# Kernel optimization log

Measured on AMD Instinct MI355X. Metric: run time of the kernel, lower is better.

The kernel has to match this reference:

```python
import jax, jax.numpy as jnp
import numpy as np

N = 512   # speakers
M = 64    # samples per speaker
D = 768   # embedding dim
EPS = 1e-8  # torch F.cosine_similarity eps


def setup_inputs() -> dict:
    key = jax.random.key(0)
    k1, = jax.random.split(key, 1)
    speaker_vectors = jax.random.normal(k1, (N * M, D), dtype=jnp.float32)
    w = jnp.asarray(10.0, dtype=jnp.float32)
    b = jnp.asarray(-5.0, dtype=jnp.float32)
    return {"speaker_vectors": speaker_vectors, "w": w, "b": b}


def _cosine(a, b):
    # torch F.cosine_similarity: a.b / (max(|a|,eps) * max(|b|,eps)), over last dim
    na = jnp.maximum(jnp.linalg.norm(a, axis=-1), EPS)
    nb = jnp.maximum(jnp.linalg.norm(b, axis=-1), EPS)
    return jnp.sum(a * b, axis=-1) / (na * nb)


def reference(speaker_vectors, w, b):
    x = speaker_vectors.reshape(N, M, D)            # [N, M, D]
    sums = x.sum(axis=1)                            # [N, D]
    centroids = sums / M                            # [N, D]
    excl = (sums[:, None, :] - x) / (M - 1)         # exclusive centroids [N, M, D]

    # cosine sim of every centroid against every sample: [N_centroid, N_spk, M]
    xn = jnp.maximum(jnp.linalg.norm(x, axis=-1), EPS)          # [N, M]
    cn = jnp.maximum(jnp.linalg.norm(centroids, axis=-1), EPS)  # [N]
    dots = jnp.einsum('nd,imd->nim', centroids, x)              # [N, N, M]
    S = w * (dots / (cn[:, None, None] * xn[None])) + b         # [N, N, M]

    # same-speaker entries use the leave-one-out centroid
    S_same = w * _cosine(excl, x) + b               # [N, M]
    idx = jnp.arange(N)
    S = S.at[idx, idx].set(S_same)                  # overwrite diagonal block

    # L_j = -S_same_j + log sum_n exp(S[n, j])
    L = -S_same + jax.scipy.special.logsumexp(S, axis=0)  # [N, M]
    return L.sum()
```

## Files before the change

kernel.cpp:

```cpp
#include <hip/hip_runtime.h>
#include <hip/hip_bf16.h>
#include <math.h>

#define EPS 1e-8f

typedef __attribute__((ext_vector_type(2))) unsigned long ulongx2;
typedef __attribute__((ext_vector_type(4))) float floatx4;
typedef unsigned char uchar_t;

#define GPTR(p) ((const __attribute__((address_space(1))) void*)(p))
#define LPTR(p) ((__attribute__((address_space(3))) void*)(p))

__device__ __forceinline__ unsigned int pk4(float a, float b, float c, float d) {
  int v = __builtin_amdgcn_cvt_pk_fp8_f32(a, b, 0, false);
  v = __builtin_amdgcn_cvt_pk_fp8_f32(c, d, v, true);
  return (unsigned int)v;
}

__global__ __launch_bounds__(512, 4) void kA(const float* __restrict__ x,
    uchar_t* __restrict__ xbf8fm, float* __restrict__ sums_f32,
    float* __restrict__ ss, float* __restrict__ rcn,
    float* __restrict__ xx, float* __restrict__ rxn,
    const float* __restrict__ wp) {
  const int n = blockIdx.x;
  const int t = threadIdx.x;
  const int wv = t >> 6, l = t & 63;
  __shared__ uchar_t xs[64][776];
  __shared__ float rqp[64][65];
  __shared__ float red8[8];

  float4 cs[3] = {{0,0,0,0},{0,0,0,0},{0,0,0,0}};
  for (int c = 0; c < 2; ++c) {
    float4 v[4][3];
#pragma unroll
    for (int rr = 0; rr < 4; ++rr) {
      const int r = wv * 8 + c * 4 + rr;
      const float* rp = x + ((size_t)n * 64 + r) * 768 + l * 4;
#pragma unroll
      for (int q = 0; q < 3; ++q) v[rr][q] = *(const float4*)(rp + q * 256);
    }
#pragma unroll
    for (int rr = 0; rr < 4; ++rr) {
      const int r = wv * 8 + c * 4 + rr;
      float rq = 0.f;
#pragma unroll
      for (int q = 0; q < 3; ++q) {
        const float4 u = v[rr][q];
        *(unsigned int*)&xs[r][l * 4 + q * 256] = pk4(u.x, u.y, u.z, u.w);
        rq += u.x*u.x + u.y*u.y + u.z*u.z + u.w*u.w;
        cs[q].x += u.x; cs[q].y += u.y; cs[q].z += u.z; cs[q].w += u.w;
      }
      rqp[r][l] = rq;
    }
  }
  __syncthreads();

  {
    const int gg = wv >> 1;
    const int half = wv & 1;
    const int g = n * 4 + gg;
#pragma unroll
    for (int ksi = 0; ksi < 6; ++ksi) {
      const int ks = half * 6 + ksi;
      const uchar_t* sp = &xs[gg * 16 + (l & 15)][ks * 64 + (l >> 4) * 8];
      uint2 lo = *(const uint2*)sp;
      uint2 hi = *(const uint2*)(sp + 32);
      uint4 outv = {lo.x, lo.y, hi.x, hi.y};
      *(uint4*)(xbf8fm + (size_t)((g * 12 + ks) * 64 + l) * 16) = outv;
    }
  }

  {
    const int r = t >> 3;
    const int o = (t & 7) * 8;
    float s = 0.f;
#pragma unroll
    for (int i = 0; i < 8; ++i) s += rqp[r][o + i];
    s += __shfl_xor(s, 1, 64);
    s += __shfl_xor(s, 2, 64);
    s += __shfl_xor(s, 4, 64);
    if ((t & 7) == 0) {
      const int j = n * 64 + r;
      xx[j] = s;
      rxn[j] = 1.0f / fmaxf(sqrtf(s), EPS);
    }
  }
  __syncthreads();

  float (*csum)[768] = (float (*)[768])&xs[0][0];
#pragma unroll
  for (int q = 0; q < 3; ++q)
    *(floatx4*)&csum[wv][l * 4 + q * 256] = (floatx4){cs[q].x, cs[q].y, cs[q].z, cs[q].w};
  __syncthreads();

  float lss = 0.f;
  {
    const int c0 = t;
    float s0 = 0.f;
#pragma unroll
    for (int w = 0; w < 8; ++w) s0 += csum[w][c0];
    sums_f32[(size_t)n * 768 + c0] = s0;
    lss += s0 * s0;
    if (t < 256) {
      const int c1 = 512 + t;
      float s1 = 0.f;
#pragma unroll
      for (int w = 0; w < 8; ++w) s1 += csum[w][c1];
      sums_f32[(size_t)n * 768 + c1] = s1;
      lss += s1 * s1;
    }
  }
  for (int o = 32; o; o >>= 1) lss += __shfl_xor(lss, o, 64);
  if (l == 0) red8[wv] = lss;
  __syncthreads();
  if (t == 0) {
    float vv = 0.f;
#pragma unroll
    for (int w = 0; w < 8; ++w) vv += red8[w];
    ss[n] = vv;
    rcn[n] = (*wp) / fmaxf(sqrtf(vv), 64.f * EPS);
  }
}

__global__ __launch_bounds__(256) void kA2(const float* __restrict__ sums_f32,
    uchar_t* __restrict__ sums8fm) {
  const int g = blockIdx.x;
  const int wv = threadIdx.x >> 6, l = threadIdx.x & 63;
#pragma unroll
  for (int ksi = 0; ksi < 3; ++ksi) {
    const int ks = wv * 3 + ksi;
    const float* sp = sums_f32 + (size_t)(g * 16 + (l & 15)) * 768
                      + ks * 64 + (l >> 4) * 8;
    float4 a0 = *(const float4*)sp;
    float4 a1 = *(const float4*)(sp + 4);
    float4 b0 = *(const float4*)(sp + 32);
    float4 b1 = *(const float4*)(sp + 36);
    uint4 outv = { pk4(a0.x, a0.y, a0.z, a0.w), pk4(a1.x, a1.y, a1.z, a1.w),
                   pk4(b0.x, b0.y, b0.z, b0.w), pk4(b1.x, b1.y, b1.z, b1.w) };
    *(uint4*)(sums8fm + (size_t)((g * 12 + ks) * 64 + l) * 16) = outv;
  }
}

__global__ __launch_bounds__(512) void kC(const uchar_t* __restrict__ xbf8fm,
    const uchar_t* __restrict__ sums8fm, const float* __restrict__ rcn,
    const float* __restrict__ rxn, float* __restrict__ colsum_part,
    float* __restrict__ sdiag_dot, const float* __restrict__ bp) {
  __shared__ uchar_t lds[2][24576];
  const int b = blockIdx.x;
  const int xcd = b & 7;
  const int inner = b >> 3;
  const int nt = inner & 3;
  const int jt = xcd + ((inner >> 2) << 3);
  const int n0 = nt * 128, j0 = jt * 256;
  const int t = threadIdx.x, wv = t >> 6, l = t & 63;
  const int wm = wv >> 2, wj = wv & 3;
  const int gA0 = n0 >> 4, gB0 = j0 >> 4;

#define STAGE(KS_, BUF_) {                                                     \
    _Pragma("unroll")                                                          \
    for (int i_ = 0; i_ < 3; ++i_) {                                           \
      const int bl_ = wv * 3 + i_;                                             \
      if (bl_ < 8) {                                                           \
        __builtin_amdgcn_global_load_lds(                                      \
            GPTR(sums8fm + (size_t)(((gA0 + bl_) * 12 + (KS_)) * 64 + l) * 16),\
            LPTR(&lds[BUF_][bl_ * 1024 + l * 16]), 16, 0, 0);                  \
      } else {                                                                 \
        __builtin_amdgcn_global_load_lds(                                      \
            GPTR(xbf8fm + (size_t)(((gB0 + bl_ - 8) * 12 + (KS_)) * 64 + l) * 16), \
            LPTR(&lds[BUF_][bl_ * 1024 + l * 16]), 16, 0, 0);                  \
      }                                                                        \
    }                                                                          \
  }

  floatx4 acc[4][4];
#pragma unroll
  for (int mi = 0; mi < 4; ++mi)
#pragma unroll
    for (int ni = 0; ni < 4; ++ni) acc[mi][ni] = (floatx4){0.f, 0.f, 0.f, 0.f};

  STAGE(0, 0)
  STAGE(1, 1)

  for (int kb = 0; kb < 12; ++kb) {
    if (kb < 11) { asm volatile("s_waitcnt vmcnt(3)" ::: "memory"); }
    else         { asm volatile("s_waitcnt vmcnt(0)" ::: "memory"); }
    __builtin_amdgcn_s_barrier();
    __builtin_amdgcn_sched_barrier(0);
    const int cb = kb & 1;

    ulongx2 af[4], bf[4];
#pragma unroll
    for (int mi = 0; mi < 4; ++mi)
      af[mi] = *(const ulongx2*)&lds[cb][(wm * 4 + mi) * 1024 + l * 16];
#pragma unroll
    for (int ni = 0; ni < 4; ++ni)
      bf[ni] = *(const ulongx2*)&lds[cb][8192 + (wj * 4 + ni) * 1024 + l * 16];
    asm volatile("s_waitcnt lgkmcnt(0)" ::: "memory");
    __builtin_amdgcn_s_barrier();
    __builtin_amdgcn_sched_barrier(0);
    if (kb + 2 < 12) STAGE(kb + 2, cb)
    __builtin_amdgcn_s_setprio(1);
#pragma unroll
    for (int mi = 0; mi < 4; ++mi)
#pragma unroll
      for (int ni = 0; ni < 4; ++ni) {
        acc[mi][ni] = __builtin_amdgcn_mfma_f32_16x16x32_fp8_fp8(
            (long)af[mi].x, (long)bf[ni].x, acc[mi][ni], 0, 0, 0);
        acc[mi][ni] = __builtin_amdgcn_mfma_f32_16x16x32_fp8_fp8(
            (long)af[mi].y, (long)bf[ni].y, acc[mi][ni], 0, 0, 0);
      }
    __builtin_amdgcn_s_setprio(0);
  }

  const float bb = *bp;
  float rxv[4], p[4] = {0.f, 0.f, 0.f, 0.f};
#pragma unroll
  for (int ni = 0; ni < 4; ++ni)
    rxv[ni] = rxn[j0 + wj * 64 + ni * 16 + (l & 15)];
  const bool diagblk = (nt == (jt >> 5));

#pragma unroll
  for (int mi = 0; mi < 4; ++mi) {
    float4 rr = *(const float4*)&rcn[n0 + wm * 64 + mi * 16 + ((l >> 4) << 2)];
    const float rc[4] = {rr.x, rr.y, rr.z, rr.w};
#pragma unroll
    for (int ni = 0; ni < 4; ++ni) {
      floatx4 a = acc[mi][ni];
#pragma unroll
      for (int q = 0; q < 4; ++q)
        p[ni] += __expf(a[q] * rc[q] * rxv[ni] + bb);
      if (diagblk) {
        const int jg = j0 + wj * 64 + ni * 16 + (l & 15);
#pragma unroll
        for (int q = 0; q < 4; ++q) {
          const int mg = n0 + wm * 64 + mi * 16 + ((l >> 4) << 2) + q;
          if (mg == (jg >> 6)) sdiag_dot[jg] = a[q];
        }
      }
    }
  }
#pragma unroll
  for (int ni = 0; ni < 4; ++ni) {
    p[ni] += __shfl_xor(p[ni], 16, 64);
    p[ni] += __shfl_xor(p[ni], 32, 64);
  }
  if (l < 16) {
    const int slot = nt * 2 + wm;
#pragma unroll
    for (int ni = 0; ni < 4; ++ni)
      colsum_part[(size_t)slot * 32768 + j0 + wj * 64 + ni * 16 + l] = p[ni];
  }
}

__global__ __launch_bounds__(256) void kD(const float* __restrict__ colsum_part,
    const float* __restrict__ sdiag_dot, const float* __restrict__ xx,
    const float* __restrict__ ss, const float* __restrict__ rcn,
    const float* __restrict__ wp, const float* __restrict__ bp,
    float* __restrict__ partial) {
  const int j = blockIdx.x * 256 + threadIdx.x;
  const int i = j >> 6;
  const float ww = *wp, bb = *bp;
  const float sx = sdiag_dot[j];
  const float xxv = xx[j];
  const float xn = fmaxf(sqrtf(xxv), EPS);
  const float rx = 1.0f / xn;
  const float sd = sx * rcn[i] * rx + bb;
  const float exn = sqrtf(fmaxf(ss[i] - 2.f * sx + xxv, 0.f)) * (1.f / 63.f);
  const float edot = (sx - xxv) * (1.f / 63.f);
  const float sm = ww * edot / (fmaxf(exn, EPS) * xn) + bb;
  float cssum = 0.f;
#pragma unroll
  for (int s = 0; s < 8; ++s) cssum += colsum_part[(size_t)s * 32768 + j];
  const float tot = cssum - __expf(sd) + __expf(sm);
  float L = -sm + logf(fmaxf(tot, 1e-30f));
  for (int o = 32; o; o >>= 1) L += __shfl_xor(L, o, 64);
  __shared__ float red[4];
  if ((threadIdx.x & 63) == 0) red[threadIdx.x >> 6] = L;
  __syncthreads();
  if (threadIdx.x == 0)
    partial[blockIdx.x] = red[0] + red[1] + red[2] + red[3];
}

__global__ __launch_bounds__(128) void kE(const float* __restrict__ partial,
    float* __restrict__ out) {
  const int t = threadIdx.x;
  float v = partial[t];
  for (int o = 32; o; o >>= 1) v += __shfl_xor(v, o, 64);
  __shared__ float r2[2];
  if ((t & 63) == 0) r2[t >> 6] = v;
  __syncthreads();
  if (t == 0) out[0] = r2[0] + r2[1];
}

extern "C" void kernel_launch(void* const* d_in, const int* in_sizes, int n_in,
                              void* d_out, int out_size, void* d_ws, size_t ws_size,
                              hipStream_t stream) {
  const float* x  = (const float*)d_in[0];
  const float* wp = (const float*)d_in[1];
  const float* bp = (const float*)d_in[2];
  float* out = (float*)d_out;

  float* fws = (float*)d_ws;
  float* ss          = fws;
  float* rcn         = fws + 512;
  float* xx          = fws + 1024;
  float* rxn         = fws + 33792;
  float* colsum_part = fws + 66560;
  float* sdiag_dot   = fws + 328704;
  float* partial     = fws + 361472;
  float* sums_f32    = fws + 361600;
  uchar_t* sums8fm   = (uchar_t*)(fws + 754816);
  uchar_t* xbf8fm    = (uchar_t*)(fws + 853120);

  kA<<<512, 512, 0, stream>>>(x, xbf8fm, sums_f32, ss, rcn, xx, rxn, wp);
  kA2<<<32, 256, 0, stream>>>(sums_f32, sums8fm);
  kC<<<512, 512, 0, stream>>>(xbf8fm, sums8fm, rcn, rxn, colsum_part, sdiag_dot, bp);
  kD<<<128, 256, 0, stream>>>(colsum_part, sdiag_dot, xx, ss, rcn, wp, bp, partial);
  kE<<<1, 128, 0, stream>>>(partial, out);
}
```

Baseline: 51.76 us.

## Switch GEMM to 32x32x64 scaled FP8 MFMA with matching fragment layout

Replaces the 16x16x32 fp8 MFMA pairs in the centroid-sample GEMM with the gfx950 32x32x64 f8f6f4 scaled MFMA using unit scales. The fragment-major fp8 layouts written by kA and kA2 are rebuilt as 32-row groups with two 1 KB halves per k-slice, and kA2 now stages rows through LDS. The epilogue is adjusted to the 32x32 accumulator layout. The goal is fewer MFMA issues and LDS reads per k-step. In exchange the wider accumulators raise register pressure, and kC gets a launch-bounds occupancy hint of 2.

```diff
diff --git a/kernel.cpp b/kernel.cpp
--- a/kernel.cpp
+++ b/kernel.cpp
@@ -4,7 +4,8 @@
 
 #define EPS 1e-8f
 
-typedef __attribute__((ext_vector_type(2))) unsigned long ulongx2;
+typedef __attribute__((ext_vector_type(8))) int intx8;
+typedef __attribute__((ext_vector_type(16))) float floatx16;
 typedef __attribute__((ext_vector_type(4))) float floatx4;
 typedef unsigned char uchar_t;
 
@@ -56,17 +57,22 @@
   __syncthreads();
 
   {
-    const int gg = wv >> 1;
-    const int half = wv & 1;
-    const int g = n * 4 + gg;
-#pragma unroll
-    for (int ksi = 0; ksi < 6; ++ksi) {
-      const int ks = half * 6 + ksi;
-      const uchar_t* sp = &xs[gg * 16 + (l & 15)][ks * 64 + (l >> 4) * 8];
-      uint2 lo = *(const uint2*)sp;
-      uint2 hi = *(const uint2*)(sp + 32);
-      uint4 outv = {lo.x, lo.y, hi.x, hi.y};
-      *(uint4*)(xbf8fm + (size_t)((g * 12 + ks) * 64 + l) * 16) = outv;
+    const int gg = wv & 1;
+    const int g = n * 2 + gg;
+    const int ks0 = (wv >> 1) * 3;
+#pragma unroll
+    for (int ksi = 0; ksi < 3; ++ksi) {
+      const int ks = ks0 + ksi;
+      const uchar_t* sp = &xs[gg * 32 + (l & 31)][ks * 64 + (l >> 5) * 32];
+      uint2 a0 = *(const uint2*)sp;
+      uint2 a1 = *(const uint2*)(sp + 8);
+      uint2 b0 = *(const uint2*)(sp + 16);
+      uint2 b1 = *(const uint2*)(sp + 24);
+      uint4 lo = {a0.x, a0.y, a1.x, a1.y};
+      uint4 hi = {b0.x, b0.y, b1.x, b1.y};
+      uchar_t* dst = xbf8fm + (size_t)(g * 12 + ks) * 2048;
+      *(uint4*)(dst + l * 16) = lo;
+      *(uint4*)(dst + 1024 + l * 16) = hi;
     }
   }
 
@@ -124,24 +130,39 @@
 
 __global__ __launch_bounds__(256) void kA2(const float* __restrict__ sums_f32,
     uchar_t* __restrict__ sums8fm) {
-  const int g = blockIdx.x;
-  const int wv = threadIdx.x >> 6, l = threadIdx.x & 63;
+  const int g0 = blockIdx.x;
+  const int t = threadIdx.x;
+  const int wv = t >> 6, l = t & 63;
+  __shared__ uchar_t xs2[32][776];
+
+  for (int r = 0; r < 8; ++r) {
+    const int row = wv * 8 + r;
+    const float* sp = sums_f32 + (size_t)(g0 * 32 + row) * 768 + l * 4;
+    float4 v0 = *(const float4*)sp;
+    float4 v1 = *(const float4*)(sp + 256);
+    float4 v2 = *(const float4*)(sp + 512);
+    *(unsigned int*)&xs2[row][l * 4]       = pk4(v0.x, v0.y, v0.z, v0.w);
+    *(unsigned int*)&xs2[row][l * 4 + 256] = pk4(v1.x, v1.y, v1.z, v1.w);
+    *(unsigned int*)&xs2[row][l * 4 + 512] = pk4(v2.x, v2.y, v2.z, v2.w);
+  }
+  __syncthreads();
 #pragma unroll
   for (int ksi = 0; ksi < 3; ++ksi) {
     const int ks = wv * 3 + ksi;
-    const float* sp = sums_f32 + (size_t)(g * 16 + (l & 15)) * 768
-                      + ks * 64 + (l >> 4) * 8;
-    float4 a0 = *(const float4*)sp;
-    float4 a1 = *(const float4*)(sp + 4);
-    float4 b0 = *(const float4*)(sp + 32);
-    float4 b1 = *(const float4*)(sp + 36);
-    uint4 outv = { pk4(a0.x, a0.y, a0.z, a0.w), pk4(a1.x, a1.y, a1.z, a1.w),
-                   pk4(b0.x, b0.y, b0.z, b0.w), pk4(b1.x, b1.y, b1.z, b1.w) };
-    *(uint4*)(sums8fm + (size_t)((g * 12 + ks) * 64 + l) * 16) = outv;
-  }
-}
-
-__global__ __launch_bounds__(512) void kC(const uchar_t* __restrict__ xbf8fm,
+    const uchar_t* sp = &xs2[l & 31][ks * 64 + (l >> 5) * 32];
+    uint2 a0 = *(const uint2*)sp;
+    uint2 a1 = *(const uint2*)(sp + 8);
+    uint2 b0 = *(const uint2*)(sp + 16);
+    uint2 b1 = *(const uint2*)(sp + 24);
+    uint4 lo = {a0.x, a0.y, a1.x, a1.y};
+    uint4 hi = {b0.x, b0.y, b1.x, b1.y};
+    uchar_t* dst = sums8fm + (size_t)(g0 * 12 + ks) * 2048;
+    *(uint4*)(dst + l * 16) = lo;
+    *(uint4*)(dst + 1024 + l * 16) = hi;
+  }
+}
+
+__global__ __launch_bounds__(512, 2) void kC(const uchar_t* __restrict__ xbf8fm,
     const uchar_t* __restrict__ sums8fm, const float* __restrict__ rcn,
     const float* __restrict__ rxn, float* __restrict__ colsum_part,
     float* __restrict__ sdiag_dot, const float* __restrict__ bp) {
@@ -154,29 +175,29 @@
   const int n0 = nt * 128, j0 = jt * 256;
   const int t = threadIdx.x, wv = t >> 6, l = t & 63;
   const int wm = wv >> 2, wj = wv & 3;
-  const int gA0 = n0 >> 4, gB0 = j0 >> 4;
+  const int gA0 = n0 >> 5, gB0 = j0 >> 5;
+  const int hi5 = l >> 5, c31 = l & 31;
 
 #define STAGE(KS_, BUF_) {                                                     \
     _Pragma("unroll")                                                          \
     for (int i_ = 0; i_ < 3; ++i_) {                                           \
-      const int bl_ = wv * 3 + i_;                                             \
-      if (bl_ < 8) {                                                           \
-        __builtin_amdgcn_global_load_lds(                                      \
-            GPTR(sums8fm + (size_t)(((gA0 + bl_) * 12 + (KS_)) * 64 + l) * 16),\
-            LPTR(&lds[BUF_][bl_ * 1024 + l * 16]), 16, 0, 0);                  \
-      } else {                                                                 \
-        __builtin_amdgcn_global_load_lds(                                      \
-            GPTR(xbf8fm + (size_t)(((gB0 + bl_ - 8) * 12 + (KS_)) * 64 + l) * 16), \
-            LPTR(&lds[BUF_][bl_ * 1024 + l * 16]), 16, 0, 0);                  \
-      }                                                                        \
+      const int li_ = wv * 3 + i_;                                             \
+      const int bi_ = li_ >> 1, hf_ = li_ & 1;                                 \
+      const uchar_t* src_ = (bi_ < 4)                                          \
+        ? sums8fm + (size_t)((gA0 + bi_) * 12 + (KS_)) * 2048 + hf_ * 1024 + l * 16 \
+        : xbf8fm + (size_t)((gB0 + bi_ - 4) * 12 + (KS_)) * 2048 + hf_ * 1024 + l * 16; \
+      __builtin_amdgcn_global_load_lds(GPTR(src_),                             \
+          LPTR(&lds[BUF_][bi_ * 2048 + hf_ * 1024]), 16, 0, 0);                \
     }                                                                          \
   }
 
-  floatx4 acc[4][4];
-#pragma unroll
-  for (int mi = 0; mi < 4; ++mi)
-#pragma unroll
-    for (int ni = 0; ni < 4; ++ni) acc[mi][ni] = (floatx4){0.f, 0.f, 0.f, 0.f};
+  floatx16 acc[2][2];
+#pragma unroll
+  for (int mi = 0; mi < 2; ++mi)
+#pragma unroll
+    for (int ni = 0; ni < 2; ++ni)
+#pragma unroll
+      for (int r = 0; r < 16; ++r) acc[mi][ni][r] = 0.f;
 
   STAGE(0, 0)
   STAGE(1, 1)
@@ -188,67 +209,71 @@
     __builtin_amdgcn_sched_barrier(0);
     const int cb = kb & 1;
 
-    ulongx2 af[4], bf[4];
-#pragma unroll
-    for (int mi = 0; mi < 4; ++mi)
-      af[mi] = *(const ulongx2*)&lds[cb][(wm * 4 + mi) * 1024 + l * 16];
-#pragma unroll
-    for (int ni = 0; ni < 4; ++ni)
-      bf[ni] = *(const ulongx2*)&lds[cb][8192 + (wj * 4 + ni) * 1024 + l * 16];
+    intx8 af[2], bf[2];
+#pragma unroll
+    for (int mi = 0; mi < 2; ++mi) {
+      const int bb_ = (wm * 2 + mi) * 2048;
+      int4 lo = *(const int4*)&lds[cb][bb_ + l * 16];
+      int4 hi = *(const int4*)&lds[cb][bb_ + 1024 + l * 16];
+      af[mi] = (intx8){lo.x, lo.y, lo.z, lo.w, hi.x, hi.y, hi.z, hi.w};
+    }
+#pragma unroll
+    for (int ni = 0; ni < 2; ++ni) {
+      const int bb_ = 8192 + (wj * 2 + ni) * 2048;
+      int4 lo = *(const int4*)&lds[cb][bb_ + l * 16];
+      int4 hi = *(const int4*)&lds[cb][bb_ + 1024 + l * 16];
+      bf[ni] = (intx8){lo.x, lo.y, lo.z, lo.w, hi.x, hi.y, hi.z, hi.w};
+    }
     asm volatile("s_waitcnt lgkmcnt(0)" ::: "memory");
     __builtin_amdgcn_s_barrier();
     __builtin_amdgcn_sched_barrier(0);
     if (kb + 2 < 12) STAGE(kb + 2, cb)
     __builtin_amdgcn_s_setprio(1);
 #pragma unroll
-    for (int mi = 0; mi < 4; ++mi)
-#pragma unroll
-      for (int ni = 0; ni < 4; ++ni) {
-        acc[mi][ni] = __builtin_amdgcn_mfma_f32_16x16x32_fp8_fp8(
-            (long)af[mi].x, (long)bf[ni].x, acc[mi][ni], 0, 0, 0);
-        acc[mi][ni] = __builtin_amdgcn_mfma_f32_16x16x32_fp8_fp8(
-            (long)af[mi].y, (long)bf[ni].y, acc[mi][ni], 0, 0, 0);
-      }
+    for (int mi = 0; mi < 2; ++mi)
+#pragma unroll
+      for (int ni = 0; ni < 2; ++ni)
+        acc[mi][ni] = __builtin_amdgcn_mfma_scale_f32_32x32x64_f8f6f4(
+            af[mi], bf[ni], acc[mi][ni], 0, 0,
+            0, 0x7F7F7F7F, 0, 0x7F7F7F7F);
     __builtin_amdgcn_s_setprio(0);
   }
 
   const float bb = *bp;
-  float rxv[4], p[4] = {0.f, 0.f, 0.f, 0.f};
-#pragma unroll
-  for (int ni = 0; ni < 4; ++ni)
-    rxv[ni] = rxn[j0 + wj * 64 + ni * 16 + (l & 15)];
+  float rxv[2], p[2] = {0.f, 0.f};
+#pragma unroll
+  for (int ni = 0; ni < 2; ++ni)
+    rxv[ni] = rxn[j0 + wj * 64 + ni * 32 + c31];
   const bool diagblk = (nt == (jt >> 5));
 
 #pragma unroll
-  for (int mi = 0; mi < 4; ++mi) {
-    float4 rr = *(const float4*)&rcn[n0 + wm * 64 + mi * 16 + ((l >> 4) << 2)];
-    const float rc[4] = {rr.x, rr.y, rr.z, rr.w};
-#pragma unroll
-    for (int ni = 0; ni < 4; ++ni) {
-      floatx4 a = acc[mi][ni];
-#pragma unroll
-      for (int q = 0; q < 4; ++q)
-        p[ni] += __expf(a[q] * rc[q] * rxv[ni] + bb);
-      if (diagblk) {
-        const int jg = j0 + wj * 64 + ni * 16 + (l & 15);
+  for (int mi = 0; mi < 2; ++mi) {
+#pragma unroll
+    for (int rq = 0; rq < 4; ++rq) {
+      float4 rr = *(const float4*)&rcn[n0 + wm * 64 + mi * 32 + rq * 8 + hi5 * 4];
+      const float rc[4] = {rr.x, rr.y, rr.z, rr.w};
+#pragma unroll
+      for (int ni = 0; ni < 2; ++ni) {
 #pragma unroll
         for (int q = 0; q < 4; ++q) {
-          const int mg = n0 + wm * 64 + mi * 16 + ((l >> 4) << 2) + q;
-          if (mg == (jg >> 6)) sdiag_dot[jg] = a[q];
+          const float a = acc[mi][ni][rq * 4 + q];
+          p[ni] += __expf(a * rc[q] * rxv[ni] + bb);
+          if (diagblk) {
+            const int jg = j0 + wj * 64 + ni * 32 + c31;
+            const int mg = n0 + wm * 64 + mi * 32 + rq * 8 + hi5 * 4 + q;
+            if (mg == (jg >> 6)) sdiag_dot[jg] = a;
+          }
         }
       }
     }
   }
 #pragma unroll
-  for (int ni = 0; ni < 4; ++ni) {
-    p[ni] += __shfl_xor(p[ni], 16, 64);
-    p[ni] += __shfl_xor(p[ni], 32, 64);
-  }
-  if (l < 16) {
+  for (int ni = 0; ni < 2; ++ni) p[ni] += __shfl_xor(p[ni], 32, 64);
+  if (l < 32) {
     const int slot = nt * 2 + wm;
 #pragma unroll
-    for (int ni = 0; ni < 4; ++ni)
-      colsum_part[(size_t)slot * 32768 + j0 + wj * 64 + ni * 16 + l] = p[ni];
+    for (int ni = 0; ni < 2; ++ni)
+      colsum_part[(size_t)slot * 32768 + j0 + wj * 64 + ni * 32 + l] = p[ni];
   }
 }
 
@@ -313,7 +338,7 @@
   uchar_t* xbf8fm    = (uchar_t*)(fws + 853120);
 
   kA<<<512, 512, 0, stream>>>(x, xbf8fm, sums_f32, ss, rcn, xx, rxn, wp);
-  kA2<<<32, 256, 0, stream>>>(sums_f32, sums8fm);
+  kA2<<<16, 256, 0, stream>>>(sums_f32, sums8fm);
   kC<<<512, 512, 0, stream>>>(xbf8fm, sums8fm, rcn, rxn, colsum_part, sdiag_dot, bp);
   kD<<<128, 256, 0, stream>>>(colsum_part, sdiag_dot, xx, ss, rcn, wp, bp, partial);
   kE<<<1, 128, 0, stream>>>(partial, out);
```

Result: slower. 93.16 us (+80.0%).
